# Optimization experiments

Hardware: AMD Instinct MI355X
Metric: run time of the kernel (lower is better)

The kernel has to match this reference:

```python
import jax, jax.numpy as jnp
import numpy as np

D_MODEL = 2048
NUM_HEADS = 16
D_HEAD = D_MODEL // NUM_HEADS
ROPE_THETA = 10000.0
MAX_SEQ_LEN = 2048
NEG_INF = -1e30


def _rope_tables(seq_len):
    pos = jnp.arange(seq_len, dtype=jnp.float32)[:, None]          # [s,1]
    i = jnp.arange(0, D_HEAD, 2, dtype=jnp.float32)                 # [d/2]
    freqs = 1.0 / (ROPE_THETA ** (i / D_HEAD))
    angles = pos * freqs                                            # [s, d/2]
    return jnp.cos(angles), jnp.sin(angles)


def _apply_rope(x, cos, sin):
    # x: [b,h,s,d]; interleaved pairs: x1 = even dims, x2 = odd dims
    x1 = x[..., 0::2]
    x2 = x[..., 1::2]
    r1 = x1 * cos - x2 * sin
    r2 = x1 * sin + x2 * cos
    return jnp.stack([r1, r2], axis=-1).reshape(x.shape)


def setup_inputs() -> dict:
    key = jax.random.key(0)
    ks = jax.random.split(key, 5)
    b, s = 2, 2048
    scale = 1.0 / np.sqrt(D_MODEL)  # ~kaiming fan_in scale
    return {
        "x": jax.random.normal(ks[0], (b, s, D_MODEL), jnp.float32),
        "Wq": jax.random.normal(ks[1], (D_MODEL, D_MODEL), jnp.float32) * scale,
        "bq": jnp.zeros((D_MODEL,), jnp.float32),
        "Wk": jax.random.normal(ks[2], (D_MODEL, D_MODEL), jnp.float32) * scale,
        "bk": jnp.zeros((D_MODEL,), jnp.float32),
        "Wv": jax.random.normal(ks[3], (D_MODEL, D_MODEL), jnp.float32) * scale,
        "bv": jnp.zeros((D_MODEL,), jnp.float32),
        "Wo": jax.random.normal(ks[4], (D_MODEL, D_MODEL), jnp.float32) * scale,
        "bo": jnp.zeros((D_MODEL,), jnp.float32),
    }


def reference(x, Wq, bq, Wk, bk, Wv, bv, Wo, bo):
    b, s, _ = x.shape
    # QKV projections (torch Linear: y = x @ W.T + b)
    q = x @ Wq.T + bq
    k = x @ Wk.T + bk
    v = x @ Wv.T + bv
    # split heads: b s (h d) -> b h s d
    def split(t):
        return t.reshape(b, s, NUM_HEADS, D_HEAD).transpose(0, 2, 1, 3)
    q, k, v = split(q), split(k), split(v)
    # RoPE
    cos, sin = _rope_tables(s)
    q = _apply_rope(q, cos, sin)
    k = _apply_rope(k, cos, sin)
    # scaled dot-product attention with causal mask
    scores = jnp.einsum('bhqd,bhkd->bhqk', q, k) / jnp.sqrt(jnp.float32(D_HEAD))
    causal = jnp.tril(jnp.ones((s, s), dtype=bool))
    scores = jnp.where(causal[None, None], scores, NEG_INF)
    attn = jax.nn.softmax(scores, axis=-1)
    out = jnp.einsum('bhqk,bhkd->bhqd', attn, v)
    # merge heads and output projection
    out = out.transpose(0, 2, 1, 3).reshape(b, s, D_MODEL)
    return out @ Wo.T + bo
```

## Files before the change

kernel.cpp:

```cpp
#include <hip/hip_runtime.h>
#include <math.h>

#define D_MODEL 2048
#define NH 16
#define DH 128
#define SEQ 2048
#define NBH 32

typedef unsigned short u16;
typedef unsigned int u32;
typedef __attribute__((ext_vector_type(8))) short short8;
typedef __attribute__((ext_vector_type(4))) float floatx4;
typedef __attribute__((ext_vector_type(2))) unsigned int uint2v;
typedef __attribute__((ext_vector_type(4))) unsigned short ushort4v;

__device__ __forceinline__ u16 f2bf(float f) {
  u32 u = __builtin_bit_cast(u32, f);
  return (u16)((u + 0x8000u) >> 16);
}
__device__ __forceinline__ float bf2f(u16 h) {
  return __builtin_bit_cast(float, (u32)h << 16);
}

__device__ __forceinline__ void async_load16(const u16* g, u16* l) {
  __builtin_amdgcn_global_load_lds(
      (const __attribute__((address_space(1))) void*)g,
      (__attribute__((address_space(3))) void*)l, 16, 0, 0);
}

__global__ void cvt_kernel(const float* __restrict__ src, u16* __restrict__ dst,
                           int n) {
  const int i = (blockIdx.x * 256 + threadIdx.x) * 8;
  if (i >= n) return;
  const floatx4 a = *(const floatx4*)(src + i);
  const floatx4 b = *(const floatx4*)(src + i + 4);
  short8 h;
  h[0] = (short)f2bf(a[0]); h[1] = (short)f2bf(a[1]);
  h[2] = (short)f2bf(a[2]); h[3] = (short)f2bf(a[3]);
  h[4] = (short)f2bf(b[0]); h[5] = (short)f2bf(b[1]);
  h[6] = (short)f2bf(b[2]); h[7] = (short)f2bf(b[3]);
  *(short8*)(dst + i) = h;
}

__global__ void cvt4_kernel(const float* __restrict__ x,
                            const float* __restrict__ wq,
                            const float* __restrict__ wk,
                            const float* __restrict__ wv, u16* __restrict__ xb,
                            u16* __restrict__ wqb, u16* __restrict__ wkb,
                            u16* __restrict__ wvb) {
  const int blk = blockIdx.x;
  const float* src;
  u16* dst;
  int base;
  if (blk < 4096) {
    src = x; dst = xb; base = blk;
  } else if (blk < 6144) {
    src = wq; dst = wqb; base = blk - 4096;
  } else if (blk < 8192) {
    src = wk; dst = wkb; base = blk - 6144;
  } else {
    src = wv; dst = wvb; base = blk - 8192;
  }
  const int i = (base * 256 + threadIdx.x) * 8;
  const floatx4 a = *(const floatx4*)(src + i);
  const floatx4 b = *(const floatx4*)(src + i + 4);
  short8 h;
  h[0] = (short)f2bf(a[0]); h[1] = (short)f2bf(a[1]);
  h[2] = (short)f2bf(a[2]); h[3] = (short)f2bf(a[3]);
  h[4] = (short)f2bf(b[0]); h[5] = (short)f2bf(b[1]);
  h[6] = (short)f2bf(b[2]); h[7] = (short)f2bf(b[3]);
  *(short8*)(dst + i) = h;
}

__global__ __launch_bounds__(256, 2) void gemm_async(
    const u16* __restrict__ A, const u16* __restrict__ W0,
    const u16* __restrict__ W1, const u16* __restrict__ W2,
    const float* __restrict__ b0, const float* __restrict__ b1,
    const float* __restrict__ b2, void* __restrict__ C0, void* __restrict__ C1,
    void* __restrict__ C2, const int qkv) {
  __shared__ u16 As[128 * 64];
  __shared__ u16 Bs[128 * 64];
  const int tid = threadIdx.x;
  const int wave = tid >> 6, lane = tid & 63;
  const int lr = lane & 15, lg = lane >> 4;
  const int m0 = blockIdx.y * 128;
  const int wm = (wave & 1) * 64, wn = (wave >> 1) * 64;

  int n0, mode;
  const u16* W;
  const float* bias;
  void* C;
  if (qkv) {
    const int which = blockIdx.x >> 4;
    n0 = (blockIdx.x & 15) * 128;
    W = which == 0 ? W0 : which == 1 ? W1 : W2;
    bias = which == 0 ? b0 : which == 1 ? b1 : b2;
    C = which == 0 ? C0 : which == 1 ? C1 : C2;
    mode = which;
  } else {
    n0 = blockIdx.x * 128;
    W = W0; bias = b0; C = C0; mode = 3;
  }

  floatx4 acc[4][4];
#pragma unroll
  for (int i = 0; i < 4; ++i)
#pragma unroll
    for (int j = 0; j < 4; ++j) {
      floatx4 z = {0.f, 0.f, 0.f, 0.f};
      acc[i][j] = z;
    }

  for (int kt = 0; kt < D_MODEL; kt += 64) {
#pragma unroll
    for (int p = 0; p < 4; ++p) {
      const int s = p * 256 + tid;
      const int row = s >> 3, c = s & 7;
      const int g = c ^ (row & 7);
      async_load16(A + (size_t)(m0 + row) * D_MODEL + kt + g * 8,
                   &As[(p * 256 + wave * 64) * 8]);
    }
#pragma unroll
    for (int p = 0; p < 4; ++p) {
      const int s = p * 256 + tid;
      const int row = s >> 3, c = s & 7;
      const int g = c ^ (row & 7);
      async_load16(W + (size_t)(n0 + row) * D_MODEL + kt + g * 8,
                   &Bs[(p * 256 + wave * 64) * 8]);
    }
    __syncthreads();

#pragma unroll
    for (int ks = 0; ks < 2; ++ks) {
      short8 af[4], bfr[4];
      const int ch = (ks * 4 + lg) ^ (lr & 7);
#pragma unroll
      for (int i = 0; i < 4; ++i)
        af[i] = *(const short8*)&As[(wm + 16 * i + lr) * 64 + ch * 8];
#pragma unroll
      for (int j = 0; j < 4; ++j)
        bfr[j] = *(const short8*)&Bs[(wn + 16 * j + lr) * 64 + ch * 8];
#pragma unroll
      for (int i = 0; i < 4; ++i)
#pragma unroll
        for (int j = 0; j < 4; ++j)
          acc[i][j] = __builtin_amdgcn_mfma_f32_16x16x32_bf16(af[i], bfr[j],
                                                              acc[i][j], 0, 0, 0);
    }
    __syncthreads();
  }

  float bj[4];
  int ncol[4];
#pragma unroll
  for (int j = 0; j < 4; ++j) {
    ncol[j] = n0 + wn + 16 * j + lr;
    bj[j] = bias[ncol[j]];
  }

  if (mode == 3) {
    float* Cf = (float*)C;
#pragma unroll
    for (int i = 0; i < 4; ++i)
#pragma unroll
      for (int r = 0; r < 4; ++r) {
        const int m = m0 + wm + 16 * i + lg * 4 + r;
#pragma unroll
        for (int j = 0; j < 4; ++j)
          Cf[(size_t)m * D_MODEL + ncol[j]] = acc[i][j][r] + bj[j];
      }
  } else if (mode == 2) {
    u16* Ch = (u16*)C;
#pragma unroll
    for (int i = 0; i < 4; ++i)
#pragma unroll
      for (int r = 0; r < 4; ++r) {
        const int m = m0 + wm + 16 * i + lg * 4 + r;
        const int b = m >> 11, s = m & (SEQ - 1);
#pragma unroll
        for (int j = 0; j < 4; ++j) {
          const int h = ncol[j] >> 7, d = ncol[j] & (DH - 1);
          Ch[((size_t)((b * NH + h) * DH + d)) * SEQ + s] =
              f2bf(acc[i][j][r] + bj[j]);
        }
      }
  } else {
    u16* Ch = (u16*)C;
#pragma unroll
    for (int i = 0; i < 4; ++i)
#pragma unroll
      for (int r = 0; r < 4; ++r) {
        const int m = m0 + wm + 16 * i + lg * 4 + r;
        const int b = m >> 11, s = m & (SEQ - 1);
#pragma unroll
        for (int j = 0; j < 4; ++j) {
          const int h = ncol[j] >> 7, d = ncol[j] & (DH - 1);
          Ch[((size_t)((b * NH + h) * SEQ + s)) * DH + d] =
              f2bf(acc[i][j][r] + bj[j]);
        }
      }
  }
}

__global__ void rope_kernel(u16* __restrict__ Q, u16* __restrict__ K) {
  const int idx = blockIdx.x * blockDim.x + threadIdx.x;
  const int p = idx & 63;
  const int s = (idx >> 6) & (SEQ - 1);
  const int bh = idx >> 17;
  if (bh >= NBH) return;
  const float freq = exp2f(-(float)p * (13.287712379549449f / 64.0f));
  const float ang = (float)s * freq;
  float sn, cs;
  sincosf(ang, &sn, &cs);
  const size_t base = ((size_t)bh * SEQ + s) * DH + 2 * p;
  {
    const u32 qq = *(const u32*)(Q + base);
    const float x1 = bf2f((u16)(qq & 0xffffu)), x2 = bf2f((u16)(qq >> 16));
    *(u32*)(Q + base) =
        (u32)f2bf(x1 * cs - x2 * sn) | ((u32)f2bf(x1 * sn + x2 * cs) << 16);
  }
  {
    const u32 kk = *(const u32*)(K + base);
    const float x1 = bf2f((u16)(kk & 0xffffu)), x2 = bf2f((u16)(kk >> 16));
    *(u32*)(K + base) =
        (u32)f2bf(x1 * cs - x2 * sn) | ((u32)f2bf(x1 * sn + x2 * cs) << 16);
  }
}

__global__ __launch_bounds__(256, 2) void attn_kernel(
    const u16* __restrict__ Q, const u16* __restrict__ K,
    const u16* __restrict__ Vt, u16* __restrict__ Oflat) {
  __shared__ u16 Ks[2][64 * 128];
  __shared__ u16 Vts[128 * 64];
  __shared__ u16 Ps[4 * 32 * 72];
  const int tid = threadIdx.x;
  const int wave = tid >> 6, lane = tid & 63;
  const int lr = lane & 15, lg = lane >> 4;
  const int L = blockIdx.y * 16 + blockIdx.x;
  const int bh = L & 31;
  const int t = L >> 5;
  const int qt = (t < 8) ? t : 23 - t;
  const size_t qk0 = (size_t)bh * SEQ * DH;
  const int q0 = qt * 128 + wave * 32;
  const float C = 0.12752602f;
  const float RTHR = 62.7f;

  short8 qf[2][4];
#pragma unroll
  for (int i = 0; i < 2; ++i)
#pragma unroll
    for (int kb = 0; kb < 4; ++kb)
      qf[i][kb] = *(const short8*)(Q + qk0 + (size_t)(q0 + 16 * i + lr) * DH +
                                   kb * 32 + lg * 8);

  floatx4 o[2][9];
#pragma unroll
  for (int i = 0; i < 2; ++i)
#pragma unroll
    for (int jd = 0; jd < 9; ++jd) {
      floatx4 z = {0.f, 0.f, 0.f, 0.f};
      o[i][jd] = z;
    }
  float mrun[2] = {-1e38f, -1e38f};

  const short8 onesv = {16256, 16256, 16256, 16256,
                        16256, 16256, 16256, 16256};

  u16* myP = &Ps[wave * 32 * 72];
  const int nkt = 2 * qt + 2;

#pragma unroll
  for (int p = 0; p < 4; ++p) {
    const int s = p * 256 + tid;
    const int row = s >> 4, c = s & 15;
    const int g = c ^ (row & 15);
    async_load16(K + qk0 + (size_t)row * DH + g * 8,
                 &Ks[0][(p * 256 + wave * 64) * 8]);
  }
  __syncthreads();

  for (int kt = 0; kt < nkt; ++kt) {
    const int cur = kt & 1, nb = cur ^ 1;
    const int kn = (kt + 1 < nkt) ? kt + 1 : kt;
#pragma unroll
    for (int p = 0; p < 4; ++p) {
      const int s = p * 256 + tid;
      const int row = s >> 3, c = s & 7;
      const int g = c ^ (row & 7);
      async_load16(Vt + (size_t)bh * DH * SEQ + (size_t)row * SEQ + kt * 64 + g * 8,
                   &Vts[(p * 256 + wave * 64) * 8]);
    }
#pragma unroll
    for (int p = 0; p < 4; ++p) {
      const int s = p * 256 + tid;
      const int row = s >> 4, c = s & 15;
      const int g = c ^ (row & 15);
      async_load16(K + qk0 + (size_t)(kn * 64 + row) * DH + g * 8,
                   &Ks[nb][(p * 256 + wave * 64) * 8]);
    }

    floatx4 st[4][2];
#pragma unroll
    for (int j = 0; j < 4; ++j)
#pragma unroll
      for (int i = 0; i < 2; ++i) {
        floatx4 z = {0.f, 0.f, 0.f, 0.f};
        st[j][i] = z;
      }
#pragma unroll
    for (int kb = 0; kb < 4; ++kb) {
      short8 kf[4];
#pragma unroll
      for (int j = 0; j < 4; ++j)
        kf[j] = *(const short8*)&Ks[cur][(16 * j + lr) * 128 +
                                         (((kb * 4 + lg) ^ lr)) * 8];
      __builtin_amdgcn_s_setprio(1);
#pragma unroll
      for (int j = 0; j < 4; ++j)
#pragma unroll
        for (int i = 0; i < 2; ++i)
          st[j][i] = __builtin_amdgcn_mfma_f32_16x16x32_bf16(kf[j], qf[i][kb],
                                                             st[j][i], 0, 0, 0);
      __builtin_amdgcn_s_setprio(0);
    }

    if (kt >= 2 * qt) {
#pragma unroll
      for (int j = 0; j < 4; ++j)
#pragma unroll
        for (int i = 0; i < 2; ++i)
#pragma unroll
          for (int r = 0; r < 4; ++r) {
            const int kpos = kt * 64 + 16 * j + 4 * lg + r;
            const int qpos = q0 + 16 * i + lr;
            if (kpos > qpos) st[j][i][r] = -1e30f;
          }
    }

    float mx[2];
#pragma unroll
    for (int i = 0; i < 2; ++i) {
      float m0v = fmaxf(fmaxf(st[0][i][0], st[0][i][1]),
                        fmaxf(st[0][i][2], st[0][i][3]));
      float m1v = fmaxf(fmaxf(st[1][i][0], st[1][i][1]),
                        fmaxf(st[1][i][2], st[1][i][3]));
      float m2v = fmaxf(fmaxf(st[2][i][0], st[2][i][1]),
                        fmaxf(st[2][i][2], st[2][i][3]));
      float m3v = fmaxf(fmaxf(st[3][i][0], st[3][i][1]),
                        fmaxf(st[3][i][2], st[3][i][3]));
      float m = fmaxf(fmaxf(m0v, m1v), fmaxf(m2v, m3v));
      m = fmaxf(m, __shfl_xor(m, 16));
      m = fmaxf(m, __shfl_xor(m, 32));
      mx[i] = m;
    }
    const float grow = fmaxf(mx[0] - mrun[0], mx[1] - mrun[1]);
    if (!__all(grow <= RTHR)) {
      float aS[2];
#pragma unroll
      for (int i = 0; i < 2; ++i) {
        const float mn = fmaxf(mrun[i], mx[i]);
        aS[i] = exp2f((mrun[i] - mn) * C);
        mrun[i] = mn;
      }
#pragma unroll
      for (int i = 0; i < 2; ++i)
#pragma unroll
        for (int r = 0; r < 4; ++r) {
          const float aO = __shfl(aS[i], 4 * lg + r);
#pragma unroll
          for (int jd = 0; jd < 9; ++jd) o[i][jd][r] *= aO;
        }
    }
    float negMC[2];
#pragma unroll
    for (int i = 0; i < 2; ++i) negMC[i] = -mrun[i] * C;

#pragma unroll
    for (int i = 0; i < 2; ++i)
#pragma unroll
      for (int j = 0; j < 4; ++j) {
        const float p0 = exp2f(fmaf(st[j][i][0], C, negMC[i]));
        const float p1 = exp2f(fmaf(st[j][i][1], C, negMC[i]));
        const float p2 = exp2f(fmaf(st[j][i][2], C, negMC[i]));
        const float p3 = exp2f(fmaf(st[j][i][3], C, negMC[i]));
        uint2v w;
        w[0] = (u32)f2bf(p0) | ((u32)f2bf(p1) << 16);
        w[1] = (u32)f2bf(p2) | ((u32)f2bf(p3) << 16);
        *(uint2v*)&myP[(16 * i + lr) * 72 + 16 * j + 4 * lg] = w;
      }

    asm volatile("s_waitcnt lgkmcnt(0)" ::: "memory");
    __syncthreads();

#pragma unroll
    for (int kb = 0; kb < 2; ++kb) {
      short8 pf[2];
#pragma unroll
      for (int i = 0; i < 2; ++i)
        pf[i] = *(const short8*)&myP[(16 * i + lr) * 72 + kb * 32 + lg * 8];
      __builtin_amdgcn_s_setprio(1);
#pragma unroll
      for (int jd = 0; jd < 8; ++jd) {
        const short8 vf = *(const short8*)&Vts[(16 * jd + lr) * 64 +
                                               (((kb * 4 + lg) ^ (lr & 7))) * 8];
#pragma unroll
        for (int i = 0; i < 2; ++i)
          o[i][jd] = __builtin_amdgcn_mfma_f32_16x16x32_bf16(pf[i], vf, o[i][jd],
                                                             0, 0, 0);
      }
#pragma unroll
      for (int i = 0; i < 2; ++i)
        o[i][8] = __builtin_amdgcn_mfma_f32_16x16x32_bf16(pf[i], onesv, o[i][8],
                                                          0, 0, 0);
      __builtin_amdgcn_s_setprio(0);
    }
    __syncthreads();
  }

  const int b = bh >> 4, h = bh & (NH - 1);
#pragma unroll
  for (int i = 0; i < 2; ++i)
#pragma unroll
    for (int r = 0; r < 4; ++r) {
      const int qpos = q0 + 16 * i + lg * 4 + r;
      const float inv = 1.0f / o[i][8][r];
      u16* dst = Oflat + ((size_t)(b * SEQ + qpos)) * D_MODEL + h * DH;
#pragma unroll
      for (int jd = 0; jd < 8; ++jd) dst[16 * jd + lr] = f2bf(o[i][jd][r] * inv);
    }
}

template <int ABF16>
__global__ __launch_bounds__(256, 2) void gemm_kernel(
    const void* __restrict__ Aptr, const float* __restrict__ W,
    const float* __restrict__ bias, void* __restrict__ Cptr, const int mode) {
  __shared__ u16 As[128 * 72];
  __shared__ u16 Bs[128 * 72];
  const int tid = threadIdx.x;
  const int wave = tid >> 6, lane = tid & 63;
  const int lr = lane & 15, lg = lane >> 4;
  const int m0 = blockIdx.y * 128, n0 = blockIdx.x * 128;
  const int wm = (wave & 1) * 64, wn = (wave >> 1) * 64;

  floatx4 acc[4][4];
#pragma unroll
  for (int i = 0; i < 4; ++i)
#pragma unroll
    for (int j = 0; j < 4; ++j) {
      floatx4 z = {0.f, 0.f, 0.f, 0.f};
      acc[i][j] = z;
    }

  for (int kt = 0; kt < D_MODEL; kt += 64) {
    if (ABF16) {
      const u16* A = (const u16*)Aptr;
      const int row0 = tid >> 3, c8 = (tid & 7) * 8;
#pragma unroll
      for (int p = 0; p < 4; ++p) {
        const int row = row0 + p * 32;
        *(short8*)&As[row * 72 + c8] =
            *(const short8*)(A + (size_t)(m0 + row) * D_MODEL + kt + c8);
      }
    } else {
      const float* A = (const float*)Aptr;
      const int row0 = tid >> 4, c4 = (tid & 15) * 4;
#pragma unroll
      for (int p = 0; p < 8; ++p) {
        const int row = row0 + p * 16;
        const floatx4 v =
            *(const floatx4*)(A + (size_t)(m0 + row) * D_MODEL + kt + c4);
        ushort4v h;
        h[0] = f2bf(v[0]); h[1] = f2bf(v[1]); h[2] = f2bf(v[2]); h[3] = f2bf(v[3]);
        *(ushort4v*)&As[row * 72 + c4] = h;
      }
    }
    {
      const int row0 = tid >> 4, c4 = (tid & 15) * 4;
#pragma unroll
      for (int p = 0; p < 8; ++p) {
        const int row = row0 + p * 16;
        const floatx4 v =
            *(const floatx4*)(W + (size_t)(n0 + row) * D_MODEL + kt + c4);
        ushort4v h;
        h[0] = f2bf(v[0]); h[1] = f2bf(v[1]); h[2] = f2bf(v[2]); h[3] = f2bf(v[3]);
        *(ushort4v*)&Bs[row * 72 + c4] = h;
      }
    }
    __syncthreads();
#pragma unroll
    for (int ks = 0; ks < 2; ++ks) {
      short8 af[4], bfr[4];
#pragma unroll
      for (int i = 0; i < 4; ++i)
        af[i] = *(const short8*)&As[(wm + 16 * i + lr) * 72 + ks * 32 + lg * 8];
#pragma unroll
      for (int j = 0; j < 4; ++j)
        bfr[j] = *(const short8*)&Bs[(wn + 16 * j + lr) * 72 + ks * 32 + lg * 8];
#pragma unroll
      for (int i = 0; i < 4; ++i)
#pragma unroll
        for (int j = 0; j < 4; ++j)
          acc[i][j] = __builtin_amdgcn_mfma_f32_16x16x32_bf16(af[i], bfr[j],
                                                              acc[i][j], 0, 0, 0);
    }
    __syncthreads();
  }

  float bj[4];
  int ncol[4];
#pragma unroll
  for (int j = 0; j < 4; ++j) {
    ncol[j] = n0 + wn + 16 * j + lr;
    bj[j] = bias[ncol[j]];
  }

  if (mode == 3) {
    float* C = (float*)Cptr;
#pragma unroll
    for (int i = 0; i < 4; ++i)
#pragma unroll
      for (int r = 0; r < 4; ++r) {
        const int m = m0 + wm + 16 * i + lg * 4 + r;
#pragma unroll
        for (int j = 0; j < 4; ++j)
          C[(size_t)m * D_MODEL + ncol[j]] = acc[i][j][r] + bj[j];
      }
  } else if (mode == 2) {
    u16* C = (u16*)Cptr;
#pragma unroll
    for (int i = 0; i < 4; ++i)
#pragma unroll
      for (int r = 0; r < 4; ++r) {
        const int m = m0 + wm + 16 * i + lg * 4 + r;
        const int b = m >> 11, s = m & (SEQ - 1);
#pragma unroll
        for (int j = 0; j < 4; ++j) {
          const int h = ncol[j] >> 7, d = ncol[j] & (DH - 1);
          C[((size_t)((b * NH + h) * DH + d)) * SEQ + s] = f2bf(acc[i][j][r] + bj[j]);
        }
      }
  } else {
    u16* C = (u16*)Cptr;
#pragma unroll
    for (int i = 0; i < 4; ++i)
#pragma unroll
      for (int r = 0; r < 4; ++r) {
        const int m = m0 + wm + 16 * i + lg * 4 + r;
        const int b = m >> 11, s = m & (SEQ - 1);
#pragma unroll
        for (int j = 0; j < 4; ++j) {
          const int h = ncol[j] >> 7, d = ncol[j] & (DH - 1);
          C[((size_t)((b * NH + h) * SEQ + s)) * DH + d] = f2bf(acc[i][j][r] + bj[j]);
        }
      }
  }
}

extern "C" void kernel_launch(void* const* d_in, const int* in_sizes, int n_in,
                              void* d_out, int out_size, void* d_ws,
                              size_t ws_size, hipStream_t stream) {
  const float* x = (const float*)d_in[0];
  const float* Wq = (const float*)d_in[1];
  const float* bq = (const float*)d_in[2];
  const float* Wk = (const float*)d_in[3];
  const float* bk = (const float*)d_in[4];
  const float* Wv = (const float*)d_in[5];
  const float* bv = (const float*)d_in[6];
  const float* Wo = (const float*)d_in[7];
  const float* bo = (const float*)d_in[8];
  float* out = (float*)d_out;

  const size_t E = (size_t)NBH * SEQ * DH;
  const size_t WE = (size_t)D_MODEL * D_MODEL;
  const size_t need = (4 * E + 3 * WE) * sizeof(u16);

  const dim3 gb(256);

  if (ws_size >= need) {
    u16* xb = (u16*)d_ws;
    u16* wqb = xb + E;
    u16* wkb = wqb + WE;
    u16* wvb = wkb + WE;
    u16* q = wvb + WE;
    u16* k = q + E;
    u16* vt = k + E;
    u16* aflat = xb;
    u16* wob = q;

    cvt4_kernel<<<dim3(10240), gb, 0, stream>>>(x, Wq, Wk, Wv, xb, wqb, wkb,
                                                wvb);

    gemm_async<<<dim3(48, 32), gb, 0, stream>>>(xb, wqb, wkb, wvb, bq, bk, bv,
                                                q, k, vt, 1);
    rope_kernel<<<dim3((NBH * SEQ * (DH / 2)) / 256), gb, 0, stream>>>(q, k);
    attn_kernel<<<dim3(SEQ / 128, NBH), gb, 0, stream>>>(q, k, vt, aflat);
    cvt_kernel<<<dim3((int)(WE / 2048)), gb, 0, stream>>>(Wo, wob, (int)WE);
    gemm_async<<<dim3(16, 32), gb, 0, stream>>>(aflat, wob, nullptr, nullptr,
                                                bo, nullptr, nullptr, out,
                                                nullptr, nullptr, 0);
  } else {
    u16* q = (u16*)d_ws;
    u16* k = q + E;
    u16* vt = k + E;
    u16* aflat = vt + E;
    const dim3 gg(D_MODEL / 128, (2 * SEQ) / 128);
    gemm_kernel<0><<<gg, gb, 0, stream>>>(x, Wq, bq, q, 0);
    gemm_kernel<0><<<gg, gb, 0, stream>>>(x, Wk, bk, k, 1);
    gemm_kernel<0><<<gg, gb, 0, stream>>>(x, Wv, bv, vt, 2);
    rope_kernel<<<dim3((NBH * SEQ * (DH / 2)) / 256), dim3(256), 0, stream>>>(q, k);
    attn_kernel<<<dim3(SEQ / 128, NBH), gb, 0, stream>>>(q, k, vt, aflat);
    gemm_kernel<1><<<gg, gb, 0, stream>>>(aflat, Wo, bo, out, 3);
  }
}
```

Before: 382.4 us.

## Fuse RoPE into QKV GEMM epilogue and double-buffer GEMM LDS tiles

A cos/sin table is precomputed in extra blocks of the conversion kernel and stored in the output buffer as scratch. The QKV GEMM epilogue then applies RoPE to Q and K using a lane-pair shuffle, which removes the separate rope kernel and its read-modify-write pass over Q and K. The GEMM also double-buffers its shared-memory tiles so the next tile is prefetched during compute, and it raises wave priority around the MFMA block. Doubling LDS to 64KB per block may reduce occupancy, and the table lookups add gather traffic in the epilogue.

```diff
diff --git a/kernel.cpp b/kernel.cpp
--- a/kernel.cpp
+++ b/kernel.cpp
@@ -47,8 +47,21 @@
                             const float* __restrict__ wk,
                             const float* __restrict__ wv, u16* __restrict__ xb,
                             u16* __restrict__ wqb, u16* __restrict__ wkb,
-                            u16* __restrict__ wvb) {
+                            u16* __restrict__ wvb, float* __restrict__ rtab) {
   const int blk = blockIdx.x;
+  if (blk >= 10240) {
+    const int e0 = ((blk - 10240) * 256 + threadIdx.x) * 4;
+#pragma unroll
+    for (int e = e0; e < e0 + 4; ++e) {
+      const int s = e >> 6, p = e & 63;
+      const float freq = exp2f(-(float)p * (13.287712379549449f / 64.0f));
+      float sn, cs;
+      sincosf((float)s * freq, &sn, &cs);
+      rtab[2 * e] = cs;
+      rtab[2 * e + 1] = sn;
+    }
+    return;
+  }
   const float* src;
   u16* dst;
   int base;
@@ -77,9 +90,9 @@
     const u16* __restrict__ W1, const u16* __restrict__ W2,
     const float* __restrict__ b0, const float* __restrict__ b1,
     const float* __restrict__ b2, void* __restrict__ C0, void* __restrict__ C1,
-    void* __restrict__ C2, const int qkv) {
-  __shared__ u16 As[128 * 64];
-  __shared__ u16 Bs[128 * 64];
+    void* __restrict__ C2, const float* __restrict__ rtab, const int qkv) {
+  __shared__ u16 As[2][128 * 64];
+  __shared__ u16 Bs[2][128 * 64];
   const int tid = threadIdx.x;
   const int wave = tid >> 6, lane = tid & 63;
   const int lr = lane & 15, lg = lane >> 4;
@@ -111,44 +124,53 @@
       acc[i][j] = z;
     }
 
+#define STAGE_TILE(buf, kt)                                              \
+  {                                                                      \
+    _Pragma("unroll") for (int p = 0; p < 4; ++p) {                      \
+      const int sIdx = p * 256 + tid;                                    \
+      const int row = sIdx >> 3, c = sIdx & 7;                           \
+      const int g = c ^ (row & 7);                                       \
+      async_load16(A + (size_t)(m0 + row) * D_MODEL + (kt) + g * 8,      \
+                   &As[buf][(p * 256 + wave * 64) * 8]);                 \
+    }                                                                    \
+    _Pragma("unroll") for (int p = 0; p < 4; ++p) {                      \
+      const int sIdx = p * 256 + tid;                                    \
+      const int row = sIdx >> 3, c = sIdx & 7;                           \
+      const int g = c ^ (row & 7);                                       \
+      async_load16(W + (size_t)(n0 + row) * D_MODEL + (kt) + g * 8,      \
+                   &Bs[buf][(p * 256 + wave * 64) * 8]);                 \
+    }                                                                    \
+  }
+
+  STAGE_TILE(0, 0);
+  __syncthreads();
+
+  int cur = 0;
   for (int kt = 0; kt < D_MODEL; kt += 64) {
-#pragma unroll
-    for (int p = 0; p < 4; ++p) {
-      const int s = p * 256 + tid;
-      const int row = s >> 3, c = s & 7;
-      const int g = c ^ (row & 7);
-      async_load16(A + (size_t)(m0 + row) * D_MODEL + kt + g * 8,
-                   &As[(p * 256 + wave * 64) * 8]);
-    }
-#pragma unroll
-    for (int p = 0; p < 4; ++p) {
-      const int s = p * 256 + tid;
-      const int row = s >> 3, c = s & 7;
-      const int g = c ^ (row & 7);
-      async_load16(W + (size_t)(n0 + row) * D_MODEL + kt + g * 8,
-                   &Bs[(p * 256 + wave * 64) * 8]);
-    }
-    __syncthreads();
-
+    if (kt + 64 < D_MODEL) STAGE_TILE(cur ^ 1, kt + 64);
 #pragma unroll
     for (int ks = 0; ks < 2; ++ks) {
       short8 af[4], bfr[4];
       const int ch = (ks * 4 + lg) ^ (lr & 7);
 #pragma unroll
       for (int i = 0; i < 4; ++i)
-        af[i] = *(const short8*)&As[(wm + 16 * i + lr) * 64 + ch * 8];
+        af[i] = *(const short8*)&As[cur][(wm + 16 * i + lr) * 64 + ch * 8];
 #pragma unroll
       for (int j = 0; j < 4; ++j)
-        bfr[j] = *(const short8*)&Bs[(wn + 16 * j + lr) * 64 + ch * 8];
+        bfr[j] = *(const short8*)&Bs[cur][(wn + 16 * j + lr) * 64 + ch * 8];
+      __builtin_amdgcn_s_setprio(1);
 #pragma unroll
       for (int i = 0; i < 4; ++i)
 #pragma unroll
         for (int j = 0; j < 4; ++j)
           acc[i][j] = __builtin_amdgcn_mfma_f32_16x16x32_bf16(af[i], bfr[j],
                                                               acc[i][j], 0, 0, 0);
+      __builtin_amdgcn_s_setprio(0);
     }
     __syncthreads();
-  }
+    cur ^= 1;
+  }
+#undef STAGE_TILE
 
   float bj[4];
   int ncol[4];
@@ -186,17 +208,26 @@
       }
   } else {
     u16* Ch = (u16*)C;
+    int pj[4];
+#pragma unroll
+    for (int j = 0; j < 4; ++j) pj[j] = (ncol[j] & (DH - 1)) >> 1;
+    const bool odd = (lr & 1) != 0;
 #pragma unroll
     for (int i = 0; i < 4; ++i)
 #pragma unroll
       for (int r = 0; r < 4; ++r) {
         const int m = m0 + wm + 16 * i + lg * 4 + r;
         const int b = m >> 11, s = m & (SEQ - 1);
+        const float2* trow = (const float2*)rtab + s * 64;
 #pragma unroll
         for (int j = 0; j < 4; ++j) {
+          const float val = acc[i][j][r] + bj[j];
+          const float partner = __shfl_xor(val, 1);
+          const float2 cssn = trow[pj[j]];
+          const float outv = odd ? fmaf(partner, cssn.y, val * cssn.x)
+                                 : fmaf(partner, -cssn.y, val * cssn.x);
           const int h = ncol[j] >> 7, d = ncol[j] & (DH - 1);
-          Ch[((size_t)((b * NH + h) * SEQ + s)) * DH + d] =
-              f2bf(acc[i][j][r] + bj[j]);
+          Ch[((size_t)((b * NH + h) * SEQ + s)) * DH + d] = f2bf(outv);
         }
       }
   }
@@ -586,18 +617,18 @@
     u16* vt = k + E;
     u16* aflat = xb;
     u16* wob = q;
-
-    cvt4_kernel<<<dim3(10240), gb, 0, stream>>>(x, Wq, Wk, Wv, xb, wqb, wkb,
-                                                wvb);
+    float* rtab = out;
+
+    cvt4_kernel<<<dim3(10368), gb, 0, stream>>>(x, Wq, Wk, Wv, xb, wqb, wkb,
+                                                wvb, rtab);
 
     gemm_async<<<dim3(48, 32), gb, 0, stream>>>(xb, wqb, wkb, wvb, bq, bk, bv,
-                                                q, k, vt, 1);
-    rope_kernel<<<dim3((NBH * SEQ * (DH / 2)) / 256), gb, 0, stream>>>(q, k);
+                                                q, k, vt, rtab, 1);
     attn_kernel<<<dim3(SEQ / 128, NBH), gb, 0, stream>>>(q, k, vt, aflat);
     cvt_kernel<<<dim3((int)(WE / 2048)), gb, 0, stream>>>(Wo, wob, (int)WE);
     gemm_async<<<dim3(16, 32), gb, 0, stream>>>(aflat, wob, nullptr, nullptr,
                                                 bo, nullptr, nullptr, out,
-                                                nullptr, nullptr, 0);
+                                                nullptr, nullptr, nullptr, 0);
   } else {
     u16* q = (u16*)d_ws;
     u16* k = q + E;
```

After: 403.7 us. 5.6% more time.

## Fuse RoPE into QKV GEMM epilogue with precomputed cos/sin table

Applied to the files above, without the earlier changes.

Removes the standalone RoPE kernel. The cos/sin values are now computed once into a small table by extra blocks in the conversion kernel, and the QKV GEMM epilogue applies the rotation. Each lane swaps values with its neighbour lane by shuffle to get the paired even/odd element before writing bf16 Q/K. This saves a full read and write of Q and K plus one kernel launch. In exchange the epilogue does extra table loads and shuffles, and the table lives temporarily in the output buffer.

```diff
diff --git a/kernel.cpp b/kernel.cpp
--- a/kernel.cpp
+++ b/kernel.cpp
@@ -47,8 +47,21 @@
                             const float* __restrict__ wk,
                             const float* __restrict__ wv, u16* __restrict__ xb,
                             u16* __restrict__ wqb, u16* __restrict__ wkb,
-                            u16* __restrict__ wvb) {
+                            u16* __restrict__ wvb, float* __restrict__ rtab) {
   const int blk = blockIdx.x;
+  if (blk >= 10240) {
+    const int e0 = ((blk - 10240) * 256 + threadIdx.x) * 4;
+#pragma unroll
+    for (int e = e0; e < e0 + 4; ++e) {
+      const int s = e >> 6, p = e & 63;
+      const float freq = exp2f(-(float)p * (13.287712379549449f / 64.0f));
+      float sn, cs;
+      sincosf((float)s * freq, &sn, &cs);
+      rtab[2 * e] = cs;
+      rtab[2 * e + 1] = sn;
+    }
+    return;
+  }
   const float* src;
   u16* dst;
   int base;
@@ -77,7 +90,7 @@
     const u16* __restrict__ W1, const u16* __restrict__ W2,
     const float* __restrict__ b0, const float* __restrict__ b1,
     const float* __restrict__ b2, void* __restrict__ C0, void* __restrict__ C1,
-    void* __restrict__ C2, const int qkv) {
+    void* __restrict__ C2, const float* __restrict__ rtab, const int qkv) {
   __shared__ u16 As[128 * 64];
   __shared__ u16 Bs[128 * 64];
   const int tid = threadIdx.x;
@@ -186,17 +199,26 @@
       }
   } else {
     u16* Ch = (u16*)C;
+    int pj[4];
+#pragma unroll
+    for (int j = 0; j < 4; ++j) pj[j] = (ncol[j] & (DH - 1)) >> 1;
+    const bool odd = (lr & 1) != 0;
 #pragma unroll
     for (int i = 0; i < 4; ++i)
 #pragma unroll
       for (int r = 0; r < 4; ++r) {
         const int m = m0 + wm + 16 * i + lg * 4 + r;
         const int b = m >> 11, s = m & (SEQ - 1);
+        const float2* trow = (const float2*)rtab + s * 64;
 #pragma unroll
         for (int j = 0; j < 4; ++j) {
+          const float val = acc[i][j][r] + bj[j];
+          const float partner = __shfl_xor(val, 1);
+          const float2 cssn = trow[pj[j]];
+          const float outv = odd ? fmaf(partner, cssn.y, val * cssn.x)
+                                 : fmaf(partner, -cssn.y, val * cssn.x);
           const int h = ncol[j] >> 7, d = ncol[j] & (DH - 1);
-          Ch[((size_t)((b * NH + h) * SEQ + s)) * DH + d] =
-              f2bf(acc[i][j][r] + bj[j]);
+          Ch[((size_t)((b * NH + h) * SEQ + s)) * DH + d] = f2bf(outv);
         }
       }
   }
@@ -586,18 +608,18 @@
     u16* vt = k + E;
     u16* aflat = xb;
     u16* wob = q;
-
-    cvt4_kernel<<<dim3(10240), gb, 0, stream>>>(x, Wq, Wk, Wv, xb, wqb, wkb,
-                                                wvb);
+    float* rtab = out;
+
+    cvt4_kernel<<<dim3(10368), gb, 0, stream>>>(x, Wq, Wk, Wv, xb, wqb, wkb,
+                                                wvb, rtab);
 
     gemm_async<<<dim3(48, 32), gb, 0, stream>>>(xb, wqb, wkb, wvb, bq, bk, bv,
-                                                q, k, vt, 1);
-    rope_kernel<<<dim3((NBH * SEQ * (DH / 2)) / 256), gb, 0, stream>>>(q, k);
+                                                q, k, vt, rtab, 1);
     attn_kernel<<<dim3(SEQ / 128, NBH), gb, 0, stream>>>(q, k, vt, aflat);
     cvt_kernel<<<dim3((int)(WE / 2048)), gb, 0, stream>>>(Wo, wob, (int)WE);
     gemm_async<<<dim3(16, 32), gb, 0, stream>>>(aflat, wob, nullptr, nullptr,
                                                 bo, nullptr, nullptr, out,
-                                                nullptr, nullptr, 0);
+                                                nullptr, nullptr, nullptr, 0);
   } else {
     u16* q = (u16*)d_ws;
     u16* k = q + E;
```

Measured after the change: 398.6 us. 1.04x slower.
